# Kernel tuning notes

Measured on AMD Instinct MI355X. Metric: run time of the kernel, lower is better.

The kernel has to match this reference:

```python
import jax, jax.numpy as jnp
import numpy as np

N, E, R, D = 100000, 300000, 2, 128


def setup_inputs() -> dict:
    key = jax.random.key(0)
    k0, k1, k2, k3, k4 = jax.random.split(key, 5)
    x = jax.random.normal(k0, (N, D), dtype=jnp.float32)
    attn_w = jax.random.normal(k1, (R, 2 * D), dtype=jnp.float32) / np.sqrt(2 * D).astype(np.float32)
    loop_weight = jax.random.normal(k2, (D, D), dtype=jnp.float32) / np.sqrt(D).astype(np.float32)
    h_bias = jnp.zeros((D,), dtype=jnp.float32)
    src = jax.random.randint(k3, (R, E), 0, N, dtype=jnp.int32)
    dst = jax.random.randint(k4, (R, E), 0, N, dtype=jnp.int32)
    return {"x": x, "attn_w": attn_w, "loop_weight": loop_weight, "h_bias": h_bias,
            "src": src, "dst": dst}


def _rel_attention(x, a, src_r, dst_r):
    # Per-edge score: attn_fc(cat(src feat, dst feat)) with Linear(2D -> 1, no bias).
    d = x.shape[1]
    xs = x[src_r]                     # [E, D] gathered source features (the messages m)
    e = xs @ a[:d] + x[dst_r] @ a[d:]  # [E] edge logits (note: no leaky_relu in message_fc path)
    # Segment (per-destination mailbox) softmax, numerically stable.
    m = jax.ops.segment_max(e, dst_r, num_segments=N)
    p = jnp.exp(e - m[dst_r])
    denom = jax.ops.segment_sum(p, dst_r, num_segments=N)
    alpha = p / jnp.maximum(denom[dst_r], jnp.float32(1e-30))  # [E]
    # Weighted scatter-sum of messages back to destination nodes.
    return jax.ops.segment_sum(alpha[:, None] * xs, dst_r, num_segments=N)  # [N, D]


def reference(x, attn_w, loop_weight, h_bias, src, dst):
    # multi_update_all(..., 'sum'): sum the per-relation attention aggregations.
    agg = _rel_attention(x, attn_w[0], src[0], dst[0])
    for r in range(1, R):
        agg = agg + _rel_attention(x, attn_w[r], src[r], dst[r])
    # self loop + bias (activation=None, dropout=0)
    h = agg + x @ loop_weight + h_bias
    return h
```

## Files before the change

### kernel.cpp

```cpp
#include <hip/hip_runtime.h>

#define N_NODES 100000
#define N_EDGES 300000
#define DIM     128
#define NBINS   (2 * N_NODES)
#define CNT_STRIDE 8
#define SLOT_CAP 24
#define ROW_TILES (N_NODES / 16)
#define GDIM (DIM + 4)
#define BATCH 8

#define WCONV_BLOCKS 8
#define BIN2_BLOCKS ((N_EDGES / 2 + 255) / 256)
#define SC_BLOCKS   1024
#define SC_WAVES    (SC_BLOCKS * 4)

typedef __attribute__((ext_vector_type(8))) short bfrag;
typedef __attribute__((ext_vector_type(4))) float f32x4;
typedef __attribute__((ext_vector_type(2))) unsigned int   u32x2;

__device__ __forceinline__ unsigned short f2bf(float f) {
  unsigned int u = __float_as_uint(f);
  u += 0x7FFFu + ((u >> 16) & 1u);
  return (unsigned short)(u >> 16);
}
__device__ __forceinline__ float bflo(unsigned int u) { return __uint_as_float(u << 16); }
__device__ __forceinline__ float bfhi(unsigned int u) { return __uint_as_float(u & 0xffff0000u); }

__global__ __launch_bounds__(256) void k1_kernel(
    const float* __restrict__ x, const float* __restrict__ attn_w,
    const float* __restrict__ W,
    const int* __restrict__ src, const int* __restrict__ dst,
    float* __restrict__ pexp, int* __restrict__ counts, int* __restrict__ slots,
    unsigned short* __restrict__ Wt, unsigned short* __restrict__ x_bf) {
  int tid = threadIdx.x;
  if (blockIdx.x < WCONV_BLOCKS) {
    for (int e = blockIdx.x * 256 + tid; e < DIM * DIM; e += WCONV_BLOCKS * 256) {
      int k = e >> 7, c = e & 127;
      Wt[c * DIM + k] = f2bf(W[e]);
    }
    return;
  }
  if (blockIdx.x < WCONV_BLOCKS + BIN2_BLOCKS) {
    int t = (blockIdx.x - WCONV_BLOCKS) * 256 + tid;
    if (t < N_EDGES / 2) {
      int ea = t, eb = t + N_EDGES / 2;
      int da0 = __builtin_nontemporal_load(&dst[ea]);
      int db0 = __builtin_nontemporal_load(&dst[eb]);
      int da1 = __builtin_nontemporal_load(&dst[ea + N_EDGES]);
      int db1 = __builtin_nontemporal_load(&dst[eb + N_EDGES]);
      int sa0 = __builtin_nontemporal_load(&src[ea]);
      int sb0 = __builtin_nontemporal_load(&src[eb]);
      int sa1 = __builtin_nontemporal_load(&src[ea + N_EDGES]);
      int sb1 = __builtin_nontemporal_load(&src[eb + N_EDGES]);
      int pa0 = atomicAdd(&counts[(size_t)(da0 * 2 + 0) * CNT_STRIDE], 1);
      int pb0 = atomicAdd(&counts[(size_t)(db0 * 2 + 0) * CNT_STRIDE], 1);
      int pa1 = atomicAdd(&counts[(size_t)(da1 * 2 + 1) * CNT_STRIDE], 1);
      int pb1 = atomicAdd(&counts[(size_t)(db1 * 2 + 1) * CNT_STRIDE], 1);
      if (pa0 < SLOT_CAP)
        __builtin_nontemporal_store(sa0, &slots[(size_t)(da0 * 2 + 0) * SLOT_CAP + pa0]);
      if (pb0 < SLOT_CAP)
        __builtin_nontemporal_store(sb0, &slots[(size_t)(db0 * 2 + 0) * SLOT_CAP + pb0]);
      if (pa1 < SLOT_CAP)
        __builtin_nontemporal_store(sa1, &slots[(size_t)(da1 * 2 + 1) * SLOT_CAP + pa1]);
      if (pb1 < SLOT_CAP)
        __builtin_nontemporal_store(sb1, &slots[(size_t)(db1 * 2 + 1) * SLOT_CAP + pb1]);
    }
    return;
  }
  int wave = (((blockIdx.x - WCONV_BLOCKS - BIN2_BLOCKS) * 256) + tid) >> 6;
  int l    = tid & 63;
  int h    = l >> 5;
  int l32  = l & 31;
  f32x4 a0 = ((const f32x4*)(attn_w +   0))[l32];
  f32x4 a1 = ((const f32x4*)(attn_w + 256))[l32];
  for (int base = wave * 2; base < N_NODES; base += SC_WAVES * 2) {
    int n = base + h;
    if (n >= N_NODES) continue;
    f32x4 v = __builtin_nontemporal_load(((const f32x4*)(x + (size_t)n * DIM)) + l32);
    unsigned int lo = ((unsigned int)f2bf(v.y) << 16) | f2bf(v.x);
    unsigned int hi = ((unsigned int)f2bf(v.w) << 16) | f2bf(v.z);
    ((u32x2*)(x_bf + (size_t)n * DIM))[l32] = (u32x2){lo, hi};
    float p0 = v.x*a0.x + v.y*a0.y + v.z*a0.z + v.w*a0.w;
    float p1 = v.x*a1.x + v.y*a1.y + v.z*a1.z + v.w*a1.w;
    #pragma unroll
    for (int off = 16; off > 0; off >>= 1) {
      p0 += __shfl_xor(p0, off, 64);
      p1 += __shfl_xor(p1, off, 64);
    }
    if (l32 == 0) {
      pexp[n]           = __expf(p0);
      pexp[N_NODES + n] = __expf(p1);
    }
  }
}

__global__ __launch_bounds__(256) void k2_kernel(
    const int* __restrict__ slots, const int* __restrict__ counts,
    const float* __restrict__ pexp, const unsigned short* __restrict__ x_bf,
    const unsigned short* __restrict__ Wt, const float* __restrict__ bias,
    float* __restrict__ out) {
  __shared__ float gtile[16][GDIM];
  int tid = threadIdx.x;
  int r0  = blockIdx.x * 16;
  int w   = tid >> 6;
  int wl  = tid & 63;
  {
    int n = wl & 15, q = wl >> 4;
    const unsigned short* xrow = x_bf + (size_t)(r0 + n) * DIM;
    f32x4 acc[2];
    #pragma unroll
    for (int c = 0; c < 2; c++) {
      float bv = bias[(2 * w + c) * 16 + n];
      acc[c] = (f32x4){bv, bv, bv, bv};
    }
    #pragma unroll
    for (int kc = 0; kc < 4; kc++) {
      int k0 = kc * 32 + q * 8;
      bfrag a = *((const bfrag*)(xrow + k0));
      #pragma unroll
      for (int c = 0; c < 2; c++) {
        bfrag b = *((const bfrag*)(Wt + (size_t)((2 * w + c) * 16 + n) * DIM + k0));
        acc[c] = __builtin_amdgcn_mfma_f32_16x16x32_bf16(a, b, acc[c], 0, 0, 0);
      }
    }
    #pragma unroll
    for (int c = 0; c < 2; c++)
      #pragma unroll
      for (int rr = 0; rr < 4; rr++)
        gtile[q * 4 + rr][(2 * w + c) * 16 + n] = acc[c][rr];
  }
  __syncthreads();
  int rrel  = wl >> 5;
  int l     = wl & 31;
  int nbase = r0 + w * 4;
  int craw[4], sraw[4];
  #pragma unroll
  for (int nn = 0; nn < 4; nn++)
    craw[nn] = __builtin_nontemporal_load(
        &counts[(size_t)((nbase + nn) * 2 + rrel) * CNT_STRIDE]);
  #pragma unroll
  for (int nn = 0; nn < 4; nn++)
    sraw[nn] = __builtin_nontemporal_load(
        &slots[(size_t)((nbase + nn) * 2 + rrel) * SLOT_CAP + l]);
  int cnt[4]; int sj[4];
  #pragma unroll
  for (int nn = 0; nn < 4; nn++) {
    cnt[nn] = (craw[nn] > SLOT_CAP) ? SLOT_CAP : craw[nn];
    sj[nn]  = (l < cnt[nn]) ? sraw[nn] : 0;
  }
  float pl[4];
  #pragma unroll
  for (int nn = 0; nn < 4; nn++)
    pl[nn] = pexp[rrel * N_NODES + sj[nn]];
  float pj[4]; float dinv[4];
  #pragma unroll
  for (int nn = 0; nn < 4; nn++) {
    pj[nn] = (l < cnt[nn]) ? pl[nn] : 0.f;
    float d = pj[nn];
    #pragma unroll
    for (int off = 16; off > 0; off >>= 1) d += __shfl_xor(d, off, 64);
    dinv[nn] = (cnt[nn] > 0) ? 1.f / d : 0.f;
  }
  u32x2 g[4][BATCH];
  #pragma unroll
  for (int u = 0; u < BATCH; u++) {
    #pragma unroll
    for (int nn = 0; nn < 4; nn++) {
      int s = __shfl(sj[nn], u, 32);
      u32x2 gv = (u32x2){0u, 0u};
      if (u < cnt[nn])
        gv = ((const u32x2*)(x_bf + (size_t)s * DIM))[l];
      g[nn][u] = gv;
    }
  }
  f32x4 accr[4];
  #pragma unroll
  for (int nn = 0; nn < 4; nn++) accr[nn] = (f32x4){0.f, 0.f, 0.f, 0.f};
  #pragma unroll
  for (int nn = 0; nn < 4; nn++) {
    #pragma unroll
    for (int u = 0; u < BATCH; u++) {
      float qv = __shfl(pj[nn], u, 32);
      u32x2 gv = g[nn][u];
      accr[nn].x += qv * bflo(gv.x);
      accr[nn].y += qv * bfhi(gv.x);
      accr[nn].z += qv * bflo(gv.y);
      accr[nn].w += qv * bfhi(gv.y);
    }
  }
  #pragma unroll
  for (int nn = 0; nn < 4; nn++) {
    int cn = cnt[nn];
    for (int j = BATCH; j < cn; j++) {
      int   s0 = __shfl(sj[nn], j, 32); float q0 = __shfl(pj[nn], j, 32);
      u32x2 g0 = ((const u32x2*)(x_bf + (size_t)s0 * DIM))[l];
      accr[nn].x += q0*bflo(g0.x); accr[nn].y += q0*bfhi(g0.x);
      accr[nn].z += q0*bflo(g0.y); accr[nn].w += q0*bfhi(g0.y);
    }
  }
  #pragma unroll
  for (int nn = 0; nn < 4; nn++) {
    f32x4 agg;
    agg.x = accr[nn].x * dinv[nn];
    agg.y = accr[nn].y * dinv[nn];
    agg.z = accr[nn].z * dinv[nn];
    agg.w = accr[nn].w * dinv[nn];
    agg.x += __shfl_xor(agg.x, 32, 64);
    agg.y += __shfl_xor(agg.y, 32, 64);
    agg.z += __shfl_xor(agg.z, 32, 64);
    agg.w += __shfl_xor(agg.w, 32, 64);
    if (wl < 32) {
      const float* gr = &gtile[w * 4 + nn][4 * wl];
      f32x4 o;
      o.x = gr[0] + agg.x; o.y = gr[1] + agg.y;
      o.z = gr[2] + agg.z; o.w = gr[3] + agg.w;
      __builtin_nontemporal_store(o, (f32x4*)(out + (size_t)(r0 + w * 4 + nn) * DIM) + wl);
    }
  }
}

extern "C" void kernel_launch(void* const* d_in, const int* in_sizes, int n_in,
                              void* d_out, int out_size, void* d_ws, size_t ws_size,
                              hipStream_t stream) {
  const float* x      = (const float*)d_in[0];
  const float* attn_w = (const float*)d_in[1];
  const float* loop_w = (const float*)d_in[2];
  const float* h_bias = (const float*)d_in[3];
  const int*   src    = (const int*)d_in[4];
  const int*   dst    = (const int*)d_in[5];
  float*       out    = (float*)d_out;

  float*          pexp   = (float*)d_ws;
  int*            counts = (int*)(pexp + NBINS);
  int*            slots  = counts + (size_t)NBINS * CNT_STRIDE;
  unsigned short* Wt     = (unsigned short*)(slots + (size_t)NBINS * SLOT_CAP);
  unsigned short* x_bf   = Wt + DIM * DIM;

  hipMemsetAsync(counts, 0, (size_t)NBINS * CNT_STRIDE * sizeof(int), stream);
  k1_kernel<<<WCONV_BLOCKS + BIN2_BLOCKS + SC_BLOCKS, 256, 0, stream>>>(
      x, attn_w, loop_w, src, dst, pexp, counts, slots, Wt, x_bf);
  k2_kernel<<<ROW_TILES, 256, 0, stream>>>(
      slots, counts, pexp, x_bf, Wt, h_bias, out);
}
```

Measured before the change: 225.4 us.

## Fuse counter zeroing with weight conversion, hoist gathers ahead of MFMA and barrier

Replaces the hipMemsetAsync of the bin counters with a small kernel that also does the weight transpose and bf16 conversion, removing that work from the binning kernel. In the aggregation kernel, the count/slot loads and the first-batch neighbor gathers are issued before the self-loop MFMA, and the barrier moves to just before the gtile read, so gather latency can overlap the matmul. BATCH drops from 8 to 4, the first-batch gathers are no longer predicated on the count (masked lanes read row 0 and are weighted by zero), and the remainder loop is unrolled by 4 to keep more loads in flight. The cost is more register pressure from values held across the MFMA section.

New measurement: 223.4 us. Within noise of the previous version (-0.9%).

```diff
diff --git a/kernel.cpp b/kernel.cpp
--- a/kernel.cpp
+++ b/kernel.cpp
@@ -8,9 +8,10 @@
 #define SLOT_CAP 24
 #define ROW_TILES (N_NODES / 16)
 #define GDIM (DIM + 4)
-#define BATCH 8
+#define BATCH 4
 
 #define WCONV_BLOCKS 8
+#define ZERO_BLOCKS ((NBINS * CNT_STRIDE / 4 + 255) / 256)
 #define BIN2_BLOCKS ((N_EDGES / 2 + 255) / 256)
 #define SC_BLOCKS   1024
 #define SC_WAVES    (SC_BLOCKS * 4)
@@ -27,22 +28,28 @@
 __device__ __forceinline__ float bflo(unsigned int u) { return __uint_as_float(u << 16); }
 __device__ __forceinline__ float bfhi(unsigned int u) { return __uint_as_float(u & 0xffff0000u); }
 
+__global__ __launch_bounds__(256) void k0_kernel(
+    int* __restrict__ counts, unsigned short* __restrict__ Wt,
+    const float* __restrict__ W) {
+  if (blockIdx.x < WCONV_BLOCKS) {
+    for (int e = blockIdx.x * 256 + threadIdx.x; e < DIM * DIM; e += WCONV_BLOCKS * 256) {
+      int k = e >> 7, c = e & 127;
+      Wt[c * DIM + k] = f2bf(W[e]);
+    }
+    return;
+  }
+  int i = (blockIdx.x - WCONV_BLOCKS) * 256 + threadIdx.x;
+  if (i < NBINS * CNT_STRIDE / 4) ((int4*)counts)[i] = make_int4(0, 0, 0, 0);
+}
+
 __global__ __launch_bounds__(256) void k1_kernel(
     const float* __restrict__ x, const float* __restrict__ attn_w,
-    const float* __restrict__ W,
     const int* __restrict__ src, const int* __restrict__ dst,
     float* __restrict__ pexp, int* __restrict__ counts, int* __restrict__ slots,
-    unsigned short* __restrict__ Wt, unsigned short* __restrict__ x_bf) {
+    unsigned short* __restrict__ x_bf) {
   int tid = threadIdx.x;
-  if (blockIdx.x < WCONV_BLOCKS) {
-    for (int e = blockIdx.x * 256 + tid; e < DIM * DIM; e += WCONV_BLOCKS * 256) {
-      int k = e >> 7, c = e & 127;
-      Wt[c * DIM + k] = f2bf(W[e]);
-    }
-    return;
-  }
-  if (blockIdx.x < WCONV_BLOCKS + BIN2_BLOCKS) {
-    int t = (blockIdx.x - WCONV_BLOCKS) * 256 + tid;
+  if (blockIdx.x < BIN2_BLOCKS) {
+    int t = blockIdx.x * 256 + tid;
     if (t < N_EDGES / 2) {
       int ea = t, eb = t + N_EDGES / 2;
       int da0 = __builtin_nontemporal_load(&dst[ea]);
@@ -68,7 +75,7 @@
     }
     return;
   }
-  int wave = (((blockIdx.x - WCONV_BLOCKS - BIN2_BLOCKS) * 256) + tid) >> 6;
+  int wave = (((blockIdx.x - BIN2_BLOCKS) * 256) + tid) >> 6;
   int l    = tid & 63;
   int h    = l >> 5;
   int l32  = l & 31;
@@ -105,6 +112,18 @@
   int r0  = blockIdx.x * 16;
   int w   = tid >> 6;
   int wl  = tid & 63;
+  int rrel  = wl >> 5;
+  int l     = wl & 31;
+  int nbase = r0 + w * 4;
+  int craw[4], sraw[4];
+  #pragma unroll
+  for (int nn = 0; nn < 4; nn++)
+    craw[nn] = __builtin_nontemporal_load(
+        &counts[(size_t)((nbase + nn) * 2 + rrel) * CNT_STRIDE]);
+  #pragma unroll
+  for (int nn = 0; nn < 4; nn++)
+    sraw[nn] = __builtin_nontemporal_load(
+        &slots[(size_t)((nbase + nn) * 2 + rrel) * SLOT_CAP + l]);
   {
     int n = wl & 15, q = wl >> 4;
     const unsigned short* xrow = x_bf + (size_t)(r0 + n) * DIM;
@@ -130,24 +149,20 @@
       for (int rr = 0; rr < 4; rr++)
         gtile[q * 4 + rr][(2 * w + c) * 16 + n] = acc[c][rr];
   }
-  __syncthreads();
-  int rrel  = wl >> 5;
-  int l     = wl & 31;
-  int nbase = r0 + w * 4;
-  int craw[4], sraw[4];
-  #pragma unroll
-  for (int nn = 0; nn < 4; nn++)
-    craw[nn] = __builtin_nontemporal_load(
-        &counts[(size_t)((nbase + nn) * 2 + rrel) * CNT_STRIDE]);
-  #pragma unroll
-  for (int nn = 0; nn < 4; nn++)
-    sraw[nn] = __builtin_nontemporal_load(
-        &slots[(size_t)((nbase + nn) * 2 + rrel) * SLOT_CAP + l]);
   int cnt[4]; int sj[4];
   #pragma unroll
   for (int nn = 0; nn < 4; nn++) {
     cnt[nn] = (craw[nn] > SLOT_CAP) ? SLOT_CAP : craw[nn];
     sj[nn]  = (l < cnt[nn]) ? sraw[nn] : 0;
+  }
+  u32x2 g[4][BATCH];
+  #pragma unroll
+  for (int u = 0; u < BATCH; u++) {
+    #pragma unroll
+    for (int nn = 0; nn < 4; nn++) {
+      int s = __shfl(sj[nn], u, 32);
+      g[nn][u] = ((const u32x2*)(x_bf + (size_t)s * DIM))[l];
+    }
   }
   float pl[4];
   #pragma unroll
@@ -161,18 +176,6 @@
     #pragma unroll
     for (int off = 16; off > 0; off >>= 1) d += __shfl_xor(d, off, 64);
     dinv[nn] = (cnt[nn] > 0) ? 1.f / d : 0.f;
-  }
-  u32x2 g[4][BATCH];
-  #pragma unroll
-  for (int u = 0; u < BATCH; u++) {
-    #pragma unroll
-    for (int nn = 0; nn < 4; nn++) {
-      int s = __shfl(sj[nn], u, 32);
-      u32x2 gv = (u32x2){0u, 0u};
-      if (u < cnt[nn])
-        gv = ((const u32x2*)(x_bf + (size_t)s * DIM))[l];
-      g[nn][u] = gv;
-    }
   }
   f32x4 accr[4];
   #pragma unroll
@@ -192,13 +195,29 @@
   #pragma unroll
   for (int nn = 0; nn < 4; nn++) {
     int cn = cnt[nn];
-    for (int j = BATCH; j < cn; j++) {
+    int j = BATCH;
+    for (; j + 4 <= cn; j += 4) {
+      int   s0 = __shfl(sj[nn], j + 0, 32); float q0 = __shfl(pj[nn], j + 0, 32);
+      int   s1 = __shfl(sj[nn], j + 1, 32); float q1 = __shfl(pj[nn], j + 1, 32);
+      int   s2 = __shfl(sj[nn], j + 2, 32); float q2 = __shfl(pj[nn], j + 2, 32);
+      int   s3 = __shfl(sj[nn], j + 3, 32); float q3 = __shfl(pj[nn], j + 3, 32);
+      u32x2 g0 = ((const u32x2*)(x_bf + (size_t)s0 * DIM))[l];
+      u32x2 g1 = ((const u32x2*)(x_bf + (size_t)s1 * DIM))[l];
+      u32x2 g2 = ((const u32x2*)(x_bf + (size_t)s2 * DIM))[l];
+      u32x2 g3 = ((const u32x2*)(x_bf + (size_t)s3 * DIM))[l];
+      accr[nn].x += q0*bflo(g0.x) + q1*bflo(g1.x) + q2*bflo(g2.x) + q3*bflo(g3.x);
+      accr[nn].y += q0*bfhi(g0.x) + q1*bfhi(g1.x) + q2*bfhi(g2.x) + q3*bfhi(g3.x);
+      accr[nn].z += q0*bflo(g0.y) + q1*bflo(g1.y) + q2*bflo(g2.y) + q3*bflo(g3.y);
+      accr[nn].w += q0*bfhi(g0.y) + q1*bfhi(g1.y) + q2*bfhi(g2.y) + q3*bfhi(g3.y);
+    }
+    for (; j < cn; j++) {
       int   s0 = __shfl(sj[nn], j, 32); float q0 = __shfl(pj[nn], j, 32);
       u32x2 g0 = ((const u32x2*)(x_bf + (size_t)s0 * DIM))[l];
       accr[nn].x += q0*bflo(g0.x); accr[nn].y += q0*bfhi(g0.x);
       accr[nn].z += q0*bflo(g0.y); accr[nn].w += q0*bfhi(g0.y);
     }
   }
+  __syncthreads();
   #pragma unroll
   for (int nn = 0; nn < 4; nn++) {
     f32x4 agg;
@@ -237,9 +256,9 @@
   unsigned short* Wt     = (unsigned short*)(slots + (size_t)NBINS * SLOT_CAP);
   unsigned short* x_bf   = Wt + DIM * DIM;
 
-  hipMemsetAsync(counts, 0, (size_t)NBINS * CNT_STRIDE * sizeof(int), stream);
-  k1_kernel<<<WCONV_BLOCKS + BIN2_BLOCKS + SC_BLOCKS, 256, 0, stream>>>(
-      x, attn_w, loop_w, src, dst, pexp, counts, slots, Wt, x_bf);
+  k0_kernel<<<WCONV_BLOCKS + ZERO_BLOCKS, 256, 0, stream>>>(counts, Wt, loop_w);
+  k1_kernel<<<BIN2_BLOCKS + SC_BLOCKS, 256, 0, stream>>>(
+      x, attn_w, src, dst, pexp, counts, slots, x_bf);
   k2_kernel<<<ROW_TILES, 256, 0, stream>>>(
       slots, counts, pexp, x_bf, Wt, h_bias, out);
 }
```
